# Optimization experiments

Measured on AMD Instinct MI355X. Metric: run time of the kernel, lower is better.

Reference implementation:

```python
import jax, jax.numpy as jnp
import numpy as np

N, E, C, S = 30000, 480000, 256, 4
T_EVO = 0.1        # evolution_time
MAX_EIG = 0.5      # max_eigenval in create_ultra_stable_hamiltonian
MAX_NORM = 0.01    # max_norm in ultra_stable_matrix_exp
MAX_TERMS = 4
LN_EPS = 1e-5


def _build_subgraphs(edge_index, n, s):
    """Emulates the per-node k_hop=1 BFS (capped at max_subgraph_size=s) and the
    subgraph laplacian Hamiltonian build (edge_weight=0.1, self-loops added).
    Pure structural preprocessing: integer/constant w.r.t. all float params."""
    src = np.asarray(edge_index[0], dtype=np.int64)
    dst = np.asarray(edge_index[1], dtype=np.int64)
    loops = np.arange(n, dtype=np.int64)
    src = np.concatenate([src, loops]); dst = np.concatenate([dst, loops])
    order = np.argsort(src, kind='stable')
    src_s, dst_s = src[order], dst[order]
    starts = np.searchsorted(src_s, np.arange(n))
    ends = np.searchsorted(src_s, np.arange(n) + 1)
    edge_set = set((src * n + dst).tolist())
    sub_nodes = np.zeros((n, s), dtype=np.int64)
    sub_mask = np.zeros((n, s), dtype=np.float32)
    H = np.zeros((n, s, s), dtype=np.float32)
    for i in range(n):
        nbrs = [i]
        for d in dst_s[starts[i]:ends[i]]:
            d = int(d)
            if d != i and d not in nbrs:
                nbrs.append(d)
                if len(nbrs) == s:
                    break
        m = len(nbrs)
        sub_nodes[i, :m] = nbrs
        sub_nodes[i, m:] = i          # pad with center (masked out below)
        sub_mask[i, :m] = 1.0
        A = np.zeros((s, s), dtype=np.float32)
        for a in range(m):
            ka = nbrs[a] * n
            for b in range(m):
                if (ka + nbrs[b]) in edge_set:
                    A[a, b] = 1.0
        deg = np.maximum(A.sum(axis=1), 1e-6)   # degree(row), clamped like torch
        H[i] = np.diag(deg) - 0.1 * A           # laplacian with edge_weight=0.1
    return sub_nodes, sub_mask, H


def _mat_fro(M):
    return jnp.sqrt(jnp.sum(jnp.abs(M) ** 2, axis=(-2, -1)))


def _unitary_from_H(sub_H):
    """ultra_stable_matrix_exp, batched over N tiny [S,S] Hamiltonians.
    The torch .item() norm/eigenvalue rescales detach gradients, so treating this
    whole block as parameter-independent (it is: H is structural) is faithful."""
    Hc = sub_H.astype(jnp.complex64)
    ev = jnp.linalg.eigvals(Hc)                              # [N,S] (CPU op)
    mx = jnp.max(ev.real, axis=-1)
    Hc = Hc * jnp.where(mx > MAX_EIG, MAX_EIG / mx, 1.0)[:, None, None]
    hn = _mat_fro(Hc)
    Hc = Hc * jnp.where(hn > MAX_NORM, MAX_NORM / hn, 1.0)[:, None, None]
    A = (-1j) * Hc * (T_EVO * 0.1)                           # scaled_H
    I = jnp.eye(S, dtype=jnp.complex64)
    U = jnp.broadcast_to(I, Hc.shape)
    term = U
    for k in range(1, MAX_TERMS + 1):
        term = jnp.matmul(term, A) / k
        tn = _mat_fro(term)
        term = term * jnp.where(tn > 0.1, 0.1 / tn, 1.0)[:, None, None]
        U = U + term
    err = _mat_fro(jnp.matmul(U, jnp.conj(jnp.swapaxes(U, -1, -2))) - I)
    U = jnp.where((err > 0.1)[:, None, None], I + A * 0.01, U)
    return U


def _cplx_linear(xr, xi, wr, wi, br, bi):
    xr = jnp.clip(xr, -10.0, 10.0); xi = jnp.clip(xi, -10.0, 10.0)
    re = xr @ wr.T - xi @ wi.T + br
    im = xr @ wi.T + xi @ wr.T + bi
    return re + 1j * im


def _cln(z, w, b, eps=LN_EPS):
    # UltraStableComplexLayerNorm, training-mode batch stats over dim 0
    mag = jnp.clip(jnp.sqrt(z.real ** 2 + z.imag ** 2 + eps), eps, 1000.0)
    mean = mag.mean(0)
    var = mag.var(0)
    nm = (mag - mean) / (jnp.sqrt(var + eps) + eps)
    sm = jnp.clip(nm * jnp.abs(w) + b, eps, 10.0)
    ph = jnp.arctan2(jnp.clip(z.imag, -1e6, 1e6), jnp.clip(z.real, -1e6, 1e6) + 1e-10)
    return sm * jnp.cos(ph) + 1j * (sm * jnp.sin(ph))


def _crelu(z, leak=0.01, mx=5.0):
    r = jnp.clip(z.real, -mx, mx); i = jnp.clip(z.imag, -mx, mx)
    return jnp.where(r > 0, r, leak * r) + 1j * jnp.where(i > 0, i, leak * i)


def setup_inputs() -> dict:
    key = jax.random.key(0)
    k1, k2, k3, k4 = jax.random.split(key, 4)
    x = jax.random.normal(k1, (N, C), dtype=jnp.float32)
    edge_index = jax.random.randint(k2, (2, E), 0, N, dtype=jnp.int64)
    sub_nodes, sub_mask, sub_H = _build_subgraphs(np.asarray(edge_index), N, S)
    std = np.sqrt(0.5 / C).astype(np.float32)
    w_real = jax.random.normal(k3, (C, C), dtype=jnp.float32) * std
    w_imag = jax.random.normal(k4, (C, C), dtype=jnp.float32) * std
    return {
        'x': x,
        'edge_index': edge_index,
        'sub_nodes': jnp.asarray(sub_nodes),
        'sub_mask': jnp.asarray(sub_mask),
        'sub_H': jnp.asarray(sub_H),
        'w_real': w_real,
        'w_imag': w_imag,
        'b_real': jnp.zeros((C,), jnp.float32),
        'b_imag': jnp.zeros((C,), jnp.float32),
        'ln_weight': jnp.full((C,), 0.1, jnp.float32),
        'ln_bias': jnp.zeros((C,), jnp.float32),
        'evolution_scale': jnp.asarray(0.1, jnp.float32),
    }


def reference(x, edge_index, sub_nodes, sub_mask, sub_H,
              w_real, w_imag, b_real, b_imag, ln_weight, ln_bias,
              evolution_scale):
    # complex linear (input is real -> imag part zero, matching torch.complex(x, 0*x))
    h = _cplx_linear(x, jnp.zeros_like(x), w_real, w_imag, b_real, b_imag)  # [N,C] c64
    U = _unitary_from_H(sub_H)                                              # [N,S,S]
    sub_x = h[sub_nodes] * sub_mask[..., None]                              # [N,S,C]
    # center node is slot 0 of each subgraph -> take row 0 of U @ sub_x
    evolved = jnp.einsum('ns,nsc->nc', U[:, 0, :], sub_x)
    out = evolved * evolution_scale + x.astype(jnp.complex64)  # residual (in==out)
    out = _cln(out, ln_weight, ln_bias)
    out = _crelu(out)
    # dropout is eval-mode identity
    return jnp.concatenate([out.real, out.imag], axis=-1)      # [N, 2C] float32
```

## Files before the change

kernel.cpp:

```cpp
#include <hip/hip_runtime.h>
#include <stdint.h>

#define N_NODES 30000
#define NC 256

typedef _Float16 f16x8 __attribute__((ext_vector_type(8)));
typedef _Float16 f16x4 __attribute__((ext_vector_type(4)));
typedef _Float16 f16x2 __attribute__((ext_vector_type(2)));
typedef float f32x4 __attribute__((ext_vector_type(4)));

#define GLOAD_LDS16(g, l) __builtin_amdgcn_global_load_lds(                      \
    (const __attribute__((address_space(1))) void*)(g),                          \
    (__attribute__((address_space(3))) void*)(l), 16, 0, 0)

#define NBX 7500
#define NBW 128
#define NBP 118
__global__ __launch_bounds__(256) void k_pre(
    const float* __restrict__ x, _Float16* __restrict__ xb,
    const float* __restrict__ wr, const float* __restrict__ wi,
    _Float16* __restrict__ Wb,
    const float* __restrict__ subH, const float* __restrict__ sub_mask,
    const float* __restrict__ escp, float* __restrict__ c4,
    float* __restrict__ ssum, float* __restrict__ ssumsq)
{
    int bid = blockIdx.x, tid = threadIdx.x;
    if (bid < NBX) {
        int i = (bid * 256 + tid) * 4;
        float4 v = *reinterpret_cast<const float4*>(x + i);
        f16x4 o;
        o[0] = (_Float16)fminf(fmaxf(v.x, -10.f), 10.f);
        o[1] = (_Float16)fminf(fmaxf(v.y, -10.f), 10.f);
        o[2] = (_Float16)fminf(fmaxf(v.z, -10.f), 10.f);
        o[3] = (_Float16)fminf(fmaxf(v.w, -10.f), 10.f);
        *reinterpret_cast<f16x4*>(xb + i) = o;
    } else if (bid < NBX + NBW) {
        int i = ((bid - NBX) * 256 + tid) * 4;
        const float* src = (i < NC * NC) ? (wr + i) : (wi + (i - NC * NC));
        float4 v = *reinterpret_cast<const float4*>(src);
        f16x4 o;
        o[0] = (_Float16)v.x; o[1] = (_Float16)v.y;
        o[2] = (_Float16)v.z; o[3] = (_Float16)v.w;
        *reinterpret_cast<f16x4*>(Wb + i) = o;
    } else if (bid < NBX + NBW + NBP) {
        int node = (bid - NBX - NBW) * 256 + tid;
        if (node < N_NODES) {
            float esc = *escp;
            const float4* Hp = reinterpret_cast<const float4*>(subH + node * 16);
            float4 r0 = Hp[0], r1 = Hp[1], r2 = Hp[2], r3 = Hp[3];
            float fr = r0.x * r0.x + r0.y * r0.y + r0.z * r0.z + r0.w * r0.w
                     + r1.x * r1.x + r1.y * r1.y + r1.z * r1.z + r1.w * r1.w
                     + r2.x * r2.x + r2.y * r2.y + r2.z * r2.z + r2.w * r2.w
                     + r3.x * r3.x + r3.y * r3.y + r3.z * r3.z + r3.w * r3.w;
            float coef = 1e-4f * rsqrtf(fr) * esc;
            float4 m = *reinterpret_cast<const float4*>(sub_mask + node * 4);
            float4 o;
            o.x = coef * r0.x * m.x;
            o.y = coef * r0.y * m.y;
            o.z = coef * r0.z * m.z;
            o.w = coef * r0.w * m.w;
            *reinterpret_cast<float4*>(c4 + node * 4) = o;
        }
    } else {
        ssum[tid] = 0.f;
        ssumsq[tid] = 0.f;
    }
}

__global__ __launch_bounds__(256, 2) void k_gemm(
    const _Float16* __restrict__ A, const _Float16* __restrict__ B,
    const float* __restrict__ br, const float* __restrict__ bi,
    _Float16* __restrict__ H)
{
    __shared__ _Float16 Bs[128 * 256];
    int bid = blockIdx.x;
    int bm = bid % 235;
    int cs = bid / 235;
    int tid = threadIdx.x;
    int wv = tid >> 6, ln = tid & 63;

#pragma unroll
    for (int i = 0; i < 16; i++) {
        int brow = i * 8 + wv * 2 + (ln >> 5);
        int chunk = ln & 31;
        int Brow = (brow < 64) ? (cs * 64 + brow) : (256 + cs * 64 + brow - 64);
        int chl = chunk ^ (brow & 7);
        const _Float16* src = B + Brow * 256 + chl * 8;
        GLOAD_LDS16(src, &Bs[i * 2048 + wv * 512]);
    }

    int quad = ln >> 4, l16 = ln & 15;
    int wm = wv >> 1, wq = wv & 1;
    int row0 = bm * 128 + wm * 64;

    const _Float16* ap[4];
#pragma unroll
    for (int mi = 0; mi < 4; mi++) {
        int r = row0 + mi * 16 + l16;
        if (r >= N_NODES) r = N_NODES - 1;
        ap[mi] = A + r * NC + quad * 8;
    }
    int brow_f[4];
#pragma unroll
    for (int ni = 0; ni < 4; ni++)
        brow_f[ni] = (ni < 2 ? 0 : 64) + wq * 32 + (ni & 1) * 16 + l16;

    __syncthreads();

    f32x4 acc[4][4] = {};
#pragma unroll
    for (int kc = 0; kc < 8; kc++) {
        f16x8 af[4];
#pragma unroll
        for (int mi = 0; mi < 4; mi++)
            af[mi] = *reinterpret_cast<const f16x8*>(ap[mi] + kc * 32);
        f16x8 bf[4];
#pragma unroll
        for (int ni = 0; ni < 4; ni++) {
            int ch = (quad + kc * 4) ^ (l16 & 7);
            bf[ni] = *reinterpret_cast<const f16x8*>(&Bs[brow_f[ni] * 256 + ch * 8]);
        }
#pragma unroll
        for (int mi = 0; mi < 4; mi++)
#pragma unroll
            for (int ni = 0; ni < 4; ni++)
                acc[mi][ni] = __builtin_amdgcn_mfma_f32_16x16x32_f16(
                    af[mi], bf[ni], acc[mi][ni], 0, 0, 0);
    }

#pragma unroll
    for (int ni = 0; ni < 2; ni++) {
        int c = cs * 64 + wq * 32 + ni * 16 + l16;
        float brc = br[c], bic = bi[c];
#pragma unroll
        for (int mi = 0; mi < 4; mi++) {
            int rowb = row0 + mi * 16 + quad * 4;
#pragma unroll
            for (int r = 0; r < 4; r++) {
                int row = rowb + r;
                if (row < N_NODES) {
                    f16x2 p;
                    p[0] = (_Float16)(acc[mi][ni][r] + brc);
                    p[1] = (_Float16)(acc[mi][ni + 2][r] + bic);
                    *reinterpret_cast<f16x2*>(H + row * 512 + 2 * c) = p;
                }
            }
        }
    }
}

#define NPB 60
#define NGRP 8
__global__ __launch_bounds__(512) void k_evolve(
    const float* __restrict__ x, const int* __restrict__ sub_nodes,
    const float* __restrict__ c4, const _Float16* __restrict__ h,
    const float* __restrict__ escp,
    float* __restrict__ outz, _Float16* __restrict__ zbuf, int use_f16,
    float* __restrict__ ssum, float* __restrict__ ssumsq)
{
    __shared__ int   s_nodes[NPB][4];
    __shared__ float s_P[NPB][4];
    __shared__ float s_redA[NGRP][256];
    __shared__ float s_redB[NGRP][256];
    int tid = threadIdx.x;
    int g = tid >> 6, lane = tid & 63;
    int base = blockIdx.x * NPB;
    if (tid < NPB) {
        int node = base + tid;
        *reinterpret_cast<float4*>(&s_P[tid][0]) =
            *reinterpret_cast<const float4*>(c4 + node * 4);
        *reinterpret_cast<int4*>(&s_nodes[tid][0]) =
            *reinterpret_cast<const int4*>(sub_nodes + node * 4);
    }
    __syncthreads();
    float esc = *escp;
    float lsum[4] = {0.f, 0.f, 0.f, 0.f};
    float lsq[4]  = {0.f, 0.f, 0.f, 0.f};

    f16x8 hvA[4];
    float4 xA;
    int j = g;
#pragma unroll
    for (int s = 0; s < 4; s++)
        hvA[s] = *reinterpret_cast<const f16x8*>(h + s_nodes[j][s] * 512 + lane * 8);
    xA = *reinterpret_cast<const float4*>(x + (base + j) * NC + lane * 4);

    for (;;) {
        int jn = j + NGRP;
        bool more = jn < NPB;
        f16x8 hvB[4];
        float4 xB;
        if (more) {
#pragma unroll
            for (int s = 0; s < 4; s++)
                hvB[s] = *reinterpret_cast<const f16x8*>(
                    h + s_nodes[jn][s] * 512 + lane * 8);
            xB = *reinterpret_cast<const float4*>(x + (base + jn) * NC + lane * 4);
        }
        {
            int node = base + j;
            float P0 = s_P[j][0], P1 = s_P[j][1], P2 = s_P[j][2], P3 = s_P[j][3];
            float xr[4] = {xA.x, xA.y, xA.z, xA.w};
            f16x8 zo;
            float or4[4], oi4[4];
#pragma unroll
            for (int e = 0; e < 4; e++) {
                float hr0 = (float)hvA[0][2 * e], hi0 = (float)hvA[0][2 * e + 1];
                float hr1 = (float)hvA[1][2 * e], hi1 = (float)hvA[1][2 * e + 1];
                float hr2 = (float)hvA[2][2 * e], hi2 = (float)hvA[2][2 * e + 1];
                float hr3 = (float)hvA[3][2 * e], hi3 = (float)hvA[3][2 * e + 1];
                float er = esc * hr0;
                float ei = esc * hi0;
                er = fmaf(P0, hi0, er); ei = fmaf(-P0, hr0, ei);
                er = fmaf(P1, hi1, er); ei = fmaf(-P1, hr1, ei);
                er = fmaf(P2, hi2, er); ei = fmaf(-P2, hr2, ei);
                er = fmaf(P3, hi3, er); ei = fmaf(-P3, hr3, ei);
                float outr = er + xr[e];
                float outi = ei;
                or4[e] = outr; oi4[e] = outi;
                zo[2 * e] = (_Float16)outr; zo[2 * e + 1] = (_Float16)outi;
                float mag = sqrtf(fmaf(outr, outr, fmaf(outi, outi, 1e-5f)));
                mag = fminf(fmaxf(mag, 1e-5f), 1000.f);
                lsum[e] += mag;
                lsq[e] = fmaf(mag, mag, lsq[e]);
            }
            if (use_f16) {
                *reinterpret_cast<f16x8*>(zbuf + node * 512 + lane * 8) = zo;
            } else {
                *reinterpret_cast<float4*>(outz + node * 512 + lane * 4) =
                    make_float4(or4[0], or4[1], or4[2], or4[3]);
                *reinterpret_cast<float4*>(outz + node * 512 + 256 + lane * 4) =
                    make_float4(oi4[0], oi4[1], oi4[2], oi4[3]);
            }
        }
        if (!more) break;
#pragma unroll
        for (int s = 0; s < 4; s++) hvA[s] = hvB[s];
        xA = xB;
        j = jn;
    }
#pragma unroll
    for (int e = 0; e < 4; e++) {
        s_redA[g][lane * 4 + e] = lsum[e];
        s_redB[g][lane * 4 + e] = lsq[e];
    }
    __syncthreads();
    if (tid < 256) {
        float a = 0.f;
#pragma unroll
        for (int q = 0; q < NGRP; q++) a += s_redA[q][tid];
        atomicAdd(&ssum[tid], a);
    } else {
        int t = tid - 256;
        float b = 0.f;
#pragma unroll
        for (int q = 0; q < NGRP; q++) b += s_redB[q][t];
        atomicAdd(&ssumsq[t], b);
    }
}

__global__ __launch_bounds__(256) void k_norm(
    float* __restrict__ out, const _Float16* __restrict__ zbuf, int use_f16,
    const float* __restrict__ ssum, const float* __restrict__ ssumsq,
    const float* __restrict__ lnw, const float* __restrict__ lnb)
{
    int tid = threadIdx.x;
    int node = blockIdx.x * 4 + (tid >> 6);
    int c0 = (tid & 63) * 4;
    float re[4], im[4];
    if (use_f16) {
        f16x8 z = *reinterpret_cast<const f16x8*>(zbuf + node * 512 + c0 * 2);
#pragma unroll
        for (int e = 0; e < 4; e++) { re[e] = (float)z[2 * e]; im[e] = (float)z[2 * e + 1]; }
    } else {
        float4 r4 = *reinterpret_cast<const float4*>(out + node * 512 + c0);
        float4 i4 = *reinterpret_cast<const float4*>(out + node * 512 + 256 + c0);
        re[0] = r4.x; re[1] = r4.y; re[2] = r4.z; re[3] = r4.w;
        im[0] = i4.x; im[1] = i4.y; im[2] = i4.z; im[3] = i4.w;
    }
    float4 s4 = *reinterpret_cast<const float4*>(ssum + c0);
    float4 q4 = *reinterpret_cast<const float4*>(ssumsq + c0);
    float4 w4 = *reinterpret_cast<const float4*>(lnw + c0);
    float4 lb4 = *reinterpret_cast<const float4*>(lnb + c0);
    float S[4] = {s4.x, s4.y, s4.z, s4.w};
    float Q[4] = {q4.x, q4.y, q4.z, q4.w};
    float W[4] = {w4.x, w4.y, w4.z, w4.w};
    float L[4] = {lb4.x, lb4.y, lb4.z, lb4.w};
    const float invN = 1.0f / (float)N_NODES;
    float orr[4], oii[4];
#pragma unroll
    for (int e = 0; e < 4; e++) {
        float mean = S[e] * invN;
        float var = fmaxf(Q[e] * invN - mean * mean, 0.f);
        float denom = sqrtf(var + 1e-5f) + 1e-5f;
        float A = fabsf(W[e]) / denom;
        float Bc = L[e] - mean * A;
        float r = re[e], i = im[e];
        float mag = sqrtf(fmaf(r, r, fmaf(i, i, 1e-5f)));
        mag = fminf(fmaxf(mag, 1e-5f), 1000.f);
        float sm = fmaf(mag, A, Bc);
        sm = fminf(fmaxf(sm, 1e-5f), 10.0f);
        float px = fminf(fmaxf(r, -1e6f), 1e6f) + 1e-10f;
        float py = fminf(fmaxf(i, -1e6f), 1e6f);
        float r2 = fmaf(px, px, py * py);
        float inv = rsqrtf(r2);
        float zr = sm * px * inv, zi = sm * py * inv;
        zr = fminf(fmaxf(zr, -5.f), 5.f);
        zi = fminf(fmaxf(zi, -5.f), 5.f);
        orr[e] = zr > 0.f ? zr : 0.01f * zr;
        oii[e] = zi > 0.f ? zi : 0.01f * zi;
    }
    *reinterpret_cast<float4*>(out + node * 512 + c0) =
        make_float4(orr[0], orr[1], orr[2], orr[3]);
    *reinterpret_cast<float4*>(out + node * 512 + 256 + c0) =
        make_float4(oii[0], oii[1], oii[2], oii[3]);
}

extern "C" void kernel_launch(void* const* d_in, const int* in_sizes, int n_in,
                              void* d_out, int out_size, void* d_ws, size_t ws_size,
                              hipStream_t stream) {
    const float* x        = (const float*)d_in[0];
    const int*   sub_nodes = (const int*)d_in[2];
    const float* sub_mask  = (const float*)d_in[3];
    const float* subH      = (const float*)d_in[4];
    const float* wr  = (const float*)d_in[5];
    const float* wi  = (const float*)d_in[6];
    const float* br  = (const float*)d_in[7];
    const float* bi  = (const float*)d_in[8];
    const float* lnw = (const float*)d_in[9];
    const float* lnb = (const float*)d_in[10];
    const float* esc = (const float*)d_in[11];
    float* out = (float*)d_out;

    char* ws = (char*)d_ws;
    const size_t XB_OFF   = 0;
    const size_t WB_OFF   = 15360000;
    const size_t H_OFF    = 15622144;
    const size_t STAT_OFF = 46342144;
    const size_t C4_OFF   = 46346240;
    const size_t ZB_OFF   = 46826240;
    const size_t WS_NEED_F16 = ZB_OFF + 30720000;
    _Float16* xb = (_Float16*)(ws + XB_OFF);
    _Float16* Wb = (_Float16*)(ws + WB_OFF);
    _Float16* h  = (_Float16*)(ws + H_OFF);
    float* ssum   = (float*)(ws + STAT_OFF);
    float* ssumsq = (float*)(ws + STAT_OFF + 1024);
    float* c4     = (float*)(ws + C4_OFF);
    _Float16* zbuf = (_Float16*)(ws + ZB_OFF);
    int use_f16 = (ws_size >= WS_NEED_F16) ? 1 : 0;

    hipLaunchKernelGGL(k_pre, dim3(NBX + NBW + NBP + 1), dim3(256), 0, stream,
                       x, xb, wr, wi, Wb, subH, sub_mask, esc, c4, ssum, ssumsq);
    hipLaunchKernelGGL(k_gemm, dim3(235 * 4), dim3(256), 0, stream, xb, Wb, br, bi, h);
    hipLaunchKernelGGL(k_evolve, dim3(500), dim3(512), 0, stream,
                       x, sub_nodes, c4, h, esc, out, zbuf, use_f16,
                       ssum, ssumsq);
    hipLaunchKernelGGL(k_norm, dim3(7500), dim3(256), 0, stream,
                       out, zbuf, use_f16, ssum, ssumsq, lnw, lnb);
}
```

Baseline: 182.3 us.

## Fuse fp32-to-fp16 conversion of x and weights into the GEMM kernel

Removes the separate preprocessing kernel and has the GEMM read x and the weight matrices directly in fp32, clamping and converting to fp16 in registers. The small per-node coefficient and stat-zeroing work moves into extra blocks of the GEMM launch. This drops one launch and the fp16 staging buffers' write and re-read. In exchange the A loads double in bytes, the B tile is loaded synchronously instead of through direct global-to-LDS loads, and each of the four column-slice blocks reconverts the same x rows.

```diff
diff --git a/kernel.cpp b/kernel.cpp
--- a/kernel.cpp
+++ b/kernel.cpp
@@ -9,96 +9,79 @@
 typedef _Float16 f16x2 __attribute__((ext_vector_type(2)));
 typedef float f32x4 __attribute__((ext_vector_type(4)));
 
-#define GLOAD_LDS16(g, l) __builtin_amdgcn_global_load_lds(                      \
-    (const __attribute__((address_space(1))) void*)(g),                          \
-    (__attribute__((address_space(3))) void*)(l), 16, 0, 0)
-
-#define NBX 7500
-#define NBW 128
-#define NBP 118
-__global__ __launch_bounds__(256) void k_pre(
-    const float* __restrict__ x, _Float16* __restrict__ xb,
-    const float* __restrict__ wr, const float* __restrict__ wi,
-    _Float16* __restrict__ Wb,
+#define NGB (235 * 4)
+#define NPREP 118
+__global__ __launch_bounds__(256, 2) void k_gemm(
+    const float* __restrict__ x, const float* __restrict__ wr,
+    const float* __restrict__ wi, const float* __restrict__ br,
+    const float* __restrict__ bi, _Float16* __restrict__ H,
     const float* __restrict__ subH, const float* __restrict__ sub_mask,
     const float* __restrict__ escp, float* __restrict__ c4,
     float* __restrict__ ssum, float* __restrict__ ssumsq)
 {
-    int bid = blockIdx.x, tid = threadIdx.x;
-    if (bid < NBX) {
-        int i = (bid * 256 + tid) * 4;
-        float4 v = *reinterpret_cast<const float4*>(x + i);
-        f16x4 o;
-        o[0] = (_Float16)fminf(fmaxf(v.x, -10.f), 10.f);
-        o[1] = (_Float16)fminf(fmaxf(v.y, -10.f), 10.f);
-        o[2] = (_Float16)fminf(fmaxf(v.z, -10.f), 10.f);
-        o[3] = (_Float16)fminf(fmaxf(v.w, -10.f), 10.f);
-        *reinterpret_cast<f16x4*>(xb + i) = o;
-    } else if (bid < NBX + NBW) {
-        int i = ((bid - NBX) * 256 + tid) * 4;
-        const float* src = (i < NC * NC) ? (wr + i) : (wi + (i - NC * NC));
-        float4 v = *reinterpret_cast<const float4*>(src);
-        f16x4 o;
-        o[0] = (_Float16)v.x; o[1] = (_Float16)v.y;
-        o[2] = (_Float16)v.z; o[3] = (_Float16)v.w;
-        *reinterpret_cast<f16x4*>(Wb + i) = o;
-    } else if (bid < NBX + NBW + NBP) {
-        int node = (bid - NBX - NBW) * 256 + tid;
-        if (node < N_NODES) {
-            float esc = *escp;
-            const float4* Hp = reinterpret_cast<const float4*>(subH + node * 16);
-            float4 r0 = Hp[0], r1 = Hp[1], r2 = Hp[2], r3 = Hp[3];
-            float fr = r0.x * r0.x + r0.y * r0.y + r0.z * r0.z + r0.w * r0.w
-                     + r1.x * r1.x + r1.y * r1.y + r1.z * r1.z + r1.w * r1.w
-                     + r2.x * r2.x + r2.y * r2.y + r2.z * r2.z + r2.w * r2.w
-                     + r3.x * r3.x + r3.y * r3.y + r3.z * r3.z + r3.w * r3.w;
-            float coef = 1e-4f * rsqrtf(fr) * esc;
-            float4 m = *reinterpret_cast<const float4*>(sub_mask + node * 4);
-            float4 o;
-            o.x = coef * r0.x * m.x;
-            o.y = coef * r0.y * m.y;
-            o.z = coef * r0.z * m.z;
-            o.w = coef * r0.w * m.w;
-            *reinterpret_cast<float4*>(c4 + node * 4) = o;
-        }
-    } else {
-        ssum[tid] = 0.f;
-        ssumsq[tid] = 0.f;
-    }
-}
-
-__global__ __launch_bounds__(256, 2) void k_gemm(
-    const _Float16* __restrict__ A, const _Float16* __restrict__ B,
-    const float* __restrict__ br, const float* __restrict__ bi,
-    _Float16* __restrict__ H)
-{
     __shared__ _Float16 Bs[128 * 256];
     int bid = blockIdx.x;
+    int tid = threadIdx.x;
+
+    if (bid >= NGB) {
+        int pb = bid - NGB;
+        if (pb < NPREP) {
+            int node = pb * 256 + tid;
+            if (node < N_NODES) {
+                float esc = *escp;
+                const float4* Hp = reinterpret_cast<const float4*>(subH + node * 16);
+                float4 r0 = Hp[0], r1 = Hp[1], r2 = Hp[2], r3 = Hp[3];
+                float fr = r0.x * r0.x + r0.y * r0.y + r0.z * r0.z + r0.w * r0.w
+                         + r1.x * r1.x + r1.y * r1.y + r1.z * r1.z + r1.w * r1.w
+                         + r2.x * r2.x + r2.y * r2.y + r2.z * r2.z + r2.w * r2.w
+                         + r3.x * r3.x + r3.y * r3.y + r3.z * r3.z + r3.w * r3.w;
+                float coef = 1e-4f * rsqrtf(fr) * esc;
+                float4 m = *reinterpret_cast<const float4*>(sub_mask + node * 4);
+                float4 o;
+                o.x = coef * r0.x * m.x;
+                o.y = coef * r0.y * m.y;
+                o.z = coef * r0.z * m.z;
+                o.w = coef * r0.w * m.w;
+                *reinterpret_cast<float4*>(c4 + node * 4) = o;
+            }
+        } else {
+            ssum[tid] = 0.f;
+            ssumsq[tid] = 0.f;
+        }
+        return;
+    }
+
     int bm = bid % 235;
     int cs = bid / 235;
-    int tid = threadIdx.x;
-    int wv = tid >> 6, ln = tid & 63;
 
 #pragma unroll
     for (int i = 0; i < 16; i++) {
-        int brow = i * 8 + wv * 2 + (ln >> 5);
-        int chunk = ln & 31;
-        int Brow = (brow < 64) ? (cs * 64 + brow) : (256 + cs * 64 + brow - 64);
-        int chl = chunk ^ (brow & 7);
-        const _Float16* src = B + Brow * 256 + chl * 8;
-        GLOAD_LDS16(src, &Bs[i * 2048 + wv * 512]);
-    }
-
+        int idx = i * 256 + tid;
+        int row = idx >> 5;
+        int lc  = idx & 31;
+        int Brow = cs * 64 + (row & 63);
+        const float* wsrc = (row < 64) ? (wr + Brow * 256) : (wi + Brow * 256);
+        float4 u = *reinterpret_cast<const float4*>(wsrc + lc * 8);
+        float4 v = *reinterpret_cast<const float4*>(wsrc + lc * 8 + 4);
+        f16x8 o;
+        o[0] = (_Float16)u.x; o[1] = (_Float16)u.y;
+        o[2] = (_Float16)u.z; o[3] = (_Float16)u.w;
+        o[4] = (_Float16)v.x; o[5] = (_Float16)v.y;
+        o[6] = (_Float16)v.z; o[7] = (_Float16)v.w;
+        *reinterpret_cast<f16x8*>(&Bs[row * 256 + (lc ^ (row & 7)) * 8]) = o;
+    }
+
+    int ln = tid & 63, wv = tid >> 6;
     int quad = ln >> 4, l16 = ln & 15;
     int wm = wv >> 1, wq = wv & 1;
     int row0 = bm * 128 + wm * 64;
 
-    const _Float16* ap[4];
+    const float* xp[4];
 #pragma unroll
     for (int mi = 0; mi < 4; mi++) {
         int r = row0 + mi * 16 + l16;
         if (r >= N_NODES) r = N_NODES - 1;
-        ap[mi] = A + r * NC + quad * 8;
+        xp[mi] = x + r * NC + quad * 8;
     }
     int brow_f[4];
 #pragma unroll
@@ -112,8 +95,20 @@
     for (int kc = 0; kc < 8; kc++) {
         f16x8 af[4];
 #pragma unroll
-        for (int mi = 0; mi < 4; mi++)
-            af[mi] = *reinterpret_cast<const f16x8*>(ap[mi] + kc * 32);
+        for (int mi = 0; mi < 4; mi++) {
+            float4 u = *reinterpret_cast<const float4*>(xp[mi] + kc * 32);
+            float4 v = *reinterpret_cast<const float4*>(xp[mi] + kc * 32 + 4);
+            f16x8 a;
+            a[0] = (_Float16)fminf(fmaxf(u.x, -10.f), 10.f);
+            a[1] = (_Float16)fminf(fmaxf(u.y, -10.f), 10.f);
+            a[2] = (_Float16)fminf(fmaxf(u.z, -10.f), 10.f);
+            a[3] = (_Float16)fminf(fmaxf(u.w, -10.f), 10.f);
+            a[4] = (_Float16)fminf(fmaxf(v.x, -10.f), 10.f);
+            a[5] = (_Float16)fminf(fmaxf(v.y, -10.f), 10.f);
+            a[6] = (_Float16)fminf(fmaxf(v.z, -10.f), 10.f);
+            a[7] = (_Float16)fminf(fmaxf(v.w, -10.f), 10.f);
+            af[mi] = a;
+        }
         f16x8 bf[4];
 #pragma unroll
         for (int ni = 0; ni < 4; ni++) {
@@ -333,15 +328,11 @@
     float* out = (float*)d_out;
 
     char* ws = (char*)d_ws;
-    const size_t XB_OFF   = 0;
-    const size_t WB_OFF   = 15360000;
-    const size_t H_OFF    = 15622144;
-    const size_t STAT_OFF = 46342144;
-    const size_t C4_OFF   = 46346240;
-    const size_t ZB_OFF   = 46826240;
+    const size_t H_OFF    = 0;
+    const size_t STAT_OFF = 30720000;
+    const size_t C4_OFF   = 30724096;
+    const size_t ZB_OFF   = 31204096;
     const size_t WS_NEED_F16 = ZB_OFF + 30720000;
-    _Float16* xb = (_Float16*)(ws + XB_OFF);
-    _Float16* Wb = (_Float16*)(ws + WB_OFF);
     _Float16* h  = (_Float16*)(ws + H_OFF);
     float* ssum   = (float*)(ws + STAT_OFF);
     float* ssumsq = (float*)(ws + STAT_OFF + 1024);
@@ -349,9 +340,9 @@
     _Float16* zbuf = (_Float16*)(ws + ZB_OFF);
     int use_f16 = (ws_size >= WS_NEED_F16) ? 1 : 0;
 
-    hipLaunchKernelGGL(k_pre, dim3(NBX + NBW + NBP + 1), dim3(256), 0, stream,
-                       x, xb, wr, wi, Wb, subH, sub_mask, esc, c4, ssum, ssumsq);
-    hipLaunchKernelGGL(k_gemm, dim3(235 * 4), dim3(256), 0, stream, xb, Wb, br, bi, h);
+    hipLaunchKernelGGL(k_gemm, dim3(NGB + NPREP + 1), dim3(256), 0, stream,
+                       x, wr, wi, br, bi, h, subH, sub_mask, esc, c4,
+                       ssum, ssumsq);
     hipLaunchKernelGGL(k_evolve, dim3(500), dim3(512), 0, stream,
                        x, sub_nodes, c4, h, esc, out, zbuf, use_f16,
                        ssum, ssumsq);
```

Result: slower. 191.0 us (+4.8%).
